# Performance work log

Measured on AMD Instinct MI355X. Metric: run time of the kernel, lower is better.

The kernel has to match this reference:

```python
import jax, jax.numpy as jnp
import numpy as np

L, B, E, H = 2048, 2, 1024, 16
HD = E // H


def setup_inputs() -> dict:
    key = jax.random.key(0)
    ks = jax.random.split(key, 5)
    s = 0.02
    return {
        "query": jax.random.normal(ks[0], (L, B, E), jnp.float32),
        "key": jax.random.normal(ks[1], (L, B, E), jnp.float32),
        "value": jax.random.normal(ks[2], (L, B, E), jnp.float32),
        "in_proj_weight": jax.random.normal(ks[3], (3 * E, E), jnp.float32) * s,
        "in_proj_bias": jnp.zeros((3 * E,), jnp.float32),
        "out_proj_weight": jax.random.normal(ks[4], (E, E), jnp.float32) * s,
        "out_proj_bias": jnp.zeros((E,), jnp.float32),
    }


def reference(query, key, value, in_proj_weight, in_proj_bias, out_proj_weight, out_proj_bias):
    # torch nn.MultiheadAttention math, seq-first [L, B, E], causal mask
    # (attend_mode='only_attend_front': positions j > i are masked).
    w_q, w_k, w_v = jnp.split(in_proj_weight, 3, axis=0)
    b_q, b_k, b_v = jnpp_split(in_proj_bias) if False else jnp.split(in_proj_bias, 3, axis=0)
    q = query @ w_q.T + b_q            # [L, B, E]
    k = key @ w_k.T + b_k
    v = value @ w_v.T + b_v

    def heads(x):  # [L, B, E] -> [B, H, L, HD]
        return x.reshape(x.shape[0], x.shape[1], H, HD).transpose(1, 2, 0, 3)

    qh, kh, vh = heads(q), heads(k), heads(v)
    scale = 1.0 / jnp.sqrt(jnp.asarray(HD, q.dtype))
    scores = jnp.einsum("bhqd,bhkd->bhqk", qh * scale, kh)  # [B, H, L, L]
    causal = jnp.triu(jnp.ones((scores.shape[-2], scores.shape[-1]), bool), k=1)
    scores = jnp.where(causal, jnp.asarray(-jnp.inf, scores.dtype), scores)
    attn = jax.nn.softmax(scores, axis=-1)
    out = jnp.einsum("bhqk,bhkd->bhqd", attn, vh)           # [B, H, L, HD]
    out = out.transpose(2, 0, 1, 3).reshape(query.shape[0], query.shape[1], E)  # [L, B, E]
    out = out @ out_proj_weight.T + out_proj_bias
    # torch also returns head-averaged attn weights [B, L, L]
    attn_avg = attn.mean(axis=1)
    return out, attn_avg
```

## Files before the change

kernel.cpp:

```cpp
#include <hip/hip_runtime.h>

#define L_ 2048
#define B_ 2
#define E_ 1024
#define H_ 16
#define HD_ 64
#define M_ 4096
#define K_ 1024

typedef unsigned short u16;
typedef unsigned int u32;
using short8  = __attribute__((ext_vector_type(8))) short;
using short4v = __attribute__((ext_vector_type(4))) short;
using floatx4 = __attribute__((ext_vector_type(4))) float;

__device__ inline u16 f2b(float f) {
  unsigned u = __float_as_uint(f);
  u += 0x7FFF + ((u >> 16) & 1);
  return (u16)(u >> 16);
}

__device__ inline u32 pack2(float a, float b) {
  u32 ua = __float_as_uint(a) + 0x8000u;
  u32 ub = __float_as_uint(b) + 0x8000u;
  return (ua >> 16) | (ub & 0xFFFF0000u);
}

__device__ inline floatx4 mfma16(short8 a, short8 b, floatx4 c) {
  return __builtin_amdgcn_mfma_f32_16x16x32_bf16(a, b, c, 0, 0, 0);
}

__device__ inline void gload16(const void* g, void* l) {
  __builtin_amdgcn_global_load_lds(
      (const __attribute__((address_space(1))) u32*)g,
      (__attribute__((address_space(3))) u32*)l, 16, 0, 0);
}

__global__ void convk(const float* __restrict__ src, u16* __restrict__ dst, int n4) {
  int i = blockIdx.x * blockDim.x + threadIdx.x;
  if (i < n4) {
    float4 v = ((const float4*)src)[i];
    ushort4 o;
    o.x = f2b(v.x); o.y = f2b(v.y); o.z = f2b(v.z); o.w = f2b(v.w);
    ((ushort4*)dst)[i] = o;
  }
}

template <int MODE>
__global__ __launch_bounds__(256) void gemm128(
    const u16* __restrict__ A, const u16* __restrict__ W, const float* __restrict__ bias,
    u16* __restrict__ qh, u16* __restrict__ kh, u16* __restrict__ vhT,
    float* __restrict__ outp)
{
  __shared__ __align__(16) u16 As[2][128 * 32];
  __shared__ __align__(16) u16 Bs[2][128 * 32];
  const int p = (MODE == 0) ? blockIdx.z : 0;
  const u16* Ap = A + (size_t)p * M_ * K_;
  const u16* Wp = W + (size_t)p * E_ * K_;
  const float* bp = bias + p * E_;
  const int row0 = blockIdx.y * 128, col0 = blockIdx.x * 128;
  const int t = threadIdx.x, lane = t & 63, wv = t >> 6;
  const int lanem = lane & 15, quad = lane >> 4;
  const int wm = wv >> 1, wn = wv & 1;

  int f0 = t, f1 = 256 + t;
  int r0s = f0 >> 2, q0s = (f0 & 3) ^ ((r0s >> 1) & 3);
  int r1s = f1 >> 2, q1s = (f1 & 3) ^ ((r1s >> 1) & 3);

  floatx4 acc[4][4];
#pragma unroll
  for (int mi = 0; mi < 4; ++mi)
#pragma unroll
    for (int ni = 0; ni < 4; ++ni) acc[mi][ni] = (floatx4){0.f, 0.f, 0.f, 0.f};

  const int swz = (lanem >> 1) & 3;

  auto STAGE = [&](int buf, int k0) {
    gload16(Ap + (size_t)(row0 + r0s) * K_ + k0 + q0s * 8, (char*)As[buf] + wv * 1024);
    gload16(Wp + (size_t)(col0 + r0s) * K_ + k0 + q0s * 8, (char*)Bs[buf] + wv * 1024);
    gload16(Ap + (size_t)(row0 + r1s) * K_ + k0 + q1s * 8, (char*)As[buf] + 4096 + wv * 1024);
    gload16(Wp + (size_t)(col0 + r1s) * K_ + k0 + q1s * 8, (char*)Bs[buf] + 4096 + wv * 1024);
  };

  STAGE(0, 0);
  for (int k0 = 0; k0 < K_; k0 += 32) {
    const int buf = (k0 >> 5) & 1;
    __syncthreads();
    if (k0 + 32 < K_) STAGE(buf ^ 1, k0 + 32);
    short8 af[4], bfg[4];
#pragma unroll
    for (int mi = 0; mi < 4; ++mi) {
      int r = wm * 64 + mi * 16 + lanem;
      af[mi] = *(const short8*)((const char*)As[buf] + r * 64 + (quad ^ swz) * 16);
    }
#pragma unroll
    for (int ni = 0; ni < 4; ++ni) {
      int r = wn * 64 + ni * 16 + lanem;
      bfg[ni] = *(const short8*)((const char*)Bs[buf] + r * 64 + (quad ^ swz) * 16);
    }
#pragma unroll
    for (int mi = 0; mi < 4; ++mi)
#pragma unroll
      for (int ni = 0; ni < 4; ++ni)
        acc[mi][ni] = mfma16(af[mi], bfg[ni], acc[mi][ni]);
  }

#pragma unroll
  for (int ni = 0; ni < 4; ++ni) {
    int gc = col0 + wn * 64 + ni * 16 + lanem;
    float bv = bp[gc];
#pragma unroll
    for (int mi = 0; mi < 4; ++mi) {
      int gr0 = row0 + wm * 64 + mi * 16 + quad * 4;
#pragma unroll
      for (int v = 0; v < 4; ++v) {
        float val = acc[mi][ni][v] + bv;
        int r = gr0 + v;
        if (MODE == 1) {
          outp[(size_t)r * E_ + gc] = val;
        } else {
          int l = r >> 1, bb = r & 1, hh = gc >> 6, d = gc & 63;
          u16 x = f2b(val);
          if (p == 0)      qh[(((size_t)bb * H_ + hh) * L_ + l) * HD_ + d] = x;
          else if (p == 1) kh[(((size_t)bb * H_ + hh) * L_ + l) * HD_ + d] = x;
          else {
            int lp = (l & ~31) | (((l >> 2) & 3) * 8 + ((l >> 4) & 1) * 4 + (l & 3));
            vhT[(((size_t)bb * H_ + hh) * HD_ + d) * L_ + lp] = x;
          }
        }
      }
    }
  }
}

__global__ __launch_bounds__(256, 2) void attn1(
    const u16* __restrict__ qh, const u16* __restrict__ kh, const u16* __restrict__ vhT,
    u16* __restrict__ ctx, float* __restrict__ li_ws)
{
  __shared__ __align__(16) u16 Ks[2][64 * 64];
  __shared__ __align__(16) u16 Vs[2][64 * 64];
  const int g = blockIdx.x;
  const int h = blockIdx.y, b = blockIdx.z;
  const int t = threadIdx.x, lane = t & 63, wv = t >> 6;
  const int lanem = lane & 15, quad = lane >> 4;
  const int bh = b * H_ + h;
  const int gB = (L_ / 64 - 1) - g;
  const int rowA = g * 64 + wv * 16 + lanem;
  const int rowB = gB * 64 + wv * 16 + lanem;

  const u16* qpA = qh + ((size_t)bh * L_ + rowA) * HD_;
  const u16* qpB = qh + ((size_t)bh * L_ + rowB) * HD_;
  short8 qA0 = *(const short8*)(qpA + quad * 8);
  short8 qA1 = *(const short8*)(qpA + 32 + quad * 8);
  short8 qB0 = *(const short8*)(qpB + quad * 8);
  short8 qB1 = *(const short8*)(qpB + 32 + quad * 8);

  const int srow = lane >> 3;
  const int spiece = (lane & 7) ^ srow;
  const u16* ksrc = kh + ((size_t)bh * L_ + wv * 16 + srow) * HD_ + spiece * 8;
  const u16* vsrc = vhT + ((size_t)bh * HD_ + wv * 16 + srow) * L_ + spiece * 8;

  const int ntiles = 32 - g;
  auto stage = [&](int buf) {
    gload16(ksrc, (char*)Ks[buf] + wv * 2048);
    gload16(ksrc + 8 * HD_, (char*)Ks[buf] + wv * 2048 + 1024);
    gload16(vsrc, (char*)Vs[buf] + wv * 2048);
    gload16(vsrc + (size_t)8 * L_, (char*)Vs[buf] + wv * 2048 + 1024);
    ksrc += 64 * HD_;
    vsrc += 64;
  };

  const int swz = lanem & 7;
  const int cb0 = lanem * 128 + ((quad ^ swz)) * 16;
  const int cb1 = lanem * 128 + ((quad ^ swz) ^ 4) * 16;

  float liA = 0.f, liB = 0.f;
  floatx4 oA[4], oB[4];
#pragma unroll
  for (int d = 0; d < 4; ++d) { oA[d] = (floatx4){0.f,0.f,0.f,0.f}; oB[d] = oA[d]; }

  int j0 = 0, tcur = 0;

  auto do_tile = [&](int modeA, int modeB) {
    __syncthreads();
    if (tcur + 1 < ntiles) stage((tcur + 1) & 1);
    const char* kbuf = (const char*)Ks[tcur & 1];
    const char* vbuf = (const char*)Vs[tcur & 1];

    floatx4 sA[4], sB[4];
#pragma unroll
    for (int jf = 0; jf < 4; ++jf) {
      short8 a0 = *(const short8*)(kbuf + cb0 + jf * 2048);
      short8 a1 = *(const short8*)(kbuf + cb1 + jf * 2048);
      floatx4 z = (floatx4){0.f,0.f,0.f,0.f};
      if (modeA != 2) sA[jf] = mfma16(a1, qA1, mfma16(a0, qA0, z));
      sB[jf] = mfma16(a1, qB1, mfma16(a0, qB0, z));
    }

    short8 pbA[2], pbB[2];
    auto soft = [&](floatx4* st, int row, float& li, short8* pb, int masked) {
#pragma unroll
      for (int jc = 0; jc < 2; ++jc) {
        float p[8];
#pragma unroll
        for (int r = 0; r < 4; ++r) {
          int ja = j0 + jc * 32 + quad * 4 + r;
          float e0 = __expf(st[jc * 2][r] * 0.125f);
          float e1 = __expf(st[jc * 2 + 1][r] * 0.125f);
          if (masked) {
            e0 = (ja <= row) ? e0 : 0.f;
            e1 = (ja + 16 <= row) ? e1 : 0.f;
          }
          li += e0 + e1;
          p[r] = e0; p[4 + r] = e1;
        }
        union { u32 w[4]; short8 s; } u;
        u.w[0] = pack2(p[0], p[1]); u.w[1] = pack2(p[2], p[3]);
        u.w[2] = pack2(p[4], p[5]); u.w[3] = pack2(p[6], p[7]);
        pb[jc] = u.s;
      }
    };
    if (modeA == 0) soft(sA, rowA, liA, pbA, 0);
    else if (modeA == 1) soft(sA, rowA, liA, pbA, 1);
    if (modeB == 0) soft(sB, rowB, liB, pbB, 0);
    else soft(sB, rowB, liB, pbB, 1);

#pragma unroll
    for (int jc = 0; jc < 2; ++jc) {
      const int base = (jc == 0) ? cb0 : cb1;
#pragma unroll
      for (int dbl = 0; dbl < 4; ++dbl) {
        short8 vf = *(const short8*)(vbuf + base + dbl * 2048);
        if (modeA != 2) oA[dbl] = mfma16(vf, pbA[jc], oA[dbl]);
        oB[dbl] = mfma16(vf, pbB[jc], oB[dbl]);
      }
    }
    j0 += 64;
    ++tcur;
  };

  stage(0);
  for (int jt = 0; jt < g; ++jt) do_tile(0, 0);
  do_tile(1, 0);
  for (int jt = g + 1; jt <= 30 - g; ++jt) do_tile(2, 0);
  do_tile(2, 1);

  liA += __shfl_xor(liA, 16); liA += __shfl_xor(liA, 32);
  liB += __shfl_xor(liB, 16); liB += __shfl_xor(liB, 32);
  float invA = 1.0f / liA, invB = 1.0f / liB;

  u16* cA = ctx + ((size_t)rowA * B_ + b) * E_ + h * HD_ + quad * 4;
  u16* cB = ctx + ((size_t)rowB * B_ + b) * E_ + h * HD_ + quad * 4;
#pragma unroll
  for (int dbl = 0; dbl < 4; ++dbl) {
    ushort4 pkA, pkB;
    pkA.x = f2b(oA[dbl][0] * invA); pkA.y = f2b(oA[dbl][1] * invA);
    pkA.z = f2b(oA[dbl][2] * invA); pkA.w = f2b(oA[dbl][3] * invA);
    pkB.x = f2b(oB[dbl][0] * invB); pkB.y = f2b(oB[dbl][1] * invB);
    pkB.z = f2b(oB[dbl][2] * invB); pkB.w = f2b(oB[dbl][3] * invB);
    *(ushort4*)(cA + dbl * 16) = pkA;
    *(ushort4*)(cB + dbl * 16) = pkB;
  }
  if (quad == 0) {
    li_ws[(size_t)bh * L_ + rowA] = invA;
    li_ws[(size_t)bh * L_ + rowB] = invB;
  }
}

__global__ __launch_bounds__(256, 2) void attn2(
    const u16* __restrict__ qh, const u16* __restrict__ kh,
    const float* __restrict__ li_ws, float* __restrict__ out2)
{
  __shared__ __align__(16) u16 Kb0[4][64 * 64];
  __shared__ __align__(16) u16 Kb1[4][64 * 64];
  const int jt = blockIdx.x, it = blockIdx.y, b = blockIdx.z;
  const int t = threadIdx.x, lane = t & 63, wv = t >> 6;
  const int lanem = lane & 15, quad = lane >> 4;
  const int j0 = jt * 64;
  const int i0 = it * 64;
  float* ob = out2 + (size_t)b * L_ * L_;

  if (jt > it) {
    float4 z = {0.f, 0.f, 0.f, 0.f};
    float* rp = ob + (size_t)(i0 + wv * 16 + lanem) * L_ + j0 + quad * 16;
    ((float4*)rp)[0] = z; ((float4*)rp)[1] = z;
    ((float4*)rp)[2] = z; ((float4*)rp)[3] = z;
    return;
  }

  const bool diag = (jt == it);
  const int srow = lane >> 3;
  const int spiece = (lane & 7) ^ srow;
  const int swz = lanem & 7;
  const int cb0 = lanem * 128 + ((quad ^ swz)) * 16;
  const int cb1 = lanem * 128 + (((4 + quad) ^ swz)) * 16;

  float acc[4][4][4] = {};

  auto STAGE = [&](u16* buf, int h) {
    const u16* kg = kh + ((size_t)(b * H_ + h) * L_ + j0) * HD_;
#pragma unroll
    for (int k = 0; k < 8; ++k)
      gload16(kg + (size_t)(k * 8 + srow) * HD_ + spiece * 8,
              (char*)buf + k * 1024);
  };

  short8 qc[4][2]; floatx4 lc[4];
  short8 qn[4][2]; floatx4 ln[4];
  auto LOADQ = [&](int h, short8 q[4][2], floatx4 l[4]) {
    const int bh = b * H_ + h;
#pragma unroll
    for (int mi = 0; mi < 4; ++mi) {
      const u16* qb = qh + ((size_t)bh * L_ + i0 + mi * 16 + lanem) * HD_;
      q[mi][0] = *(const short8*)(qb + quad * 8);
      q[mi][1] = *(const short8*)(qb + 32 + quad * 8);
      l[mi] = *(const floatx4*)(li_ws + (size_t)bh * L_ + i0 + mi * 16 + quad * 4);
    }
  };

  auto COMPUTE = [&](const u16* buf) {
#pragma unroll
    for (int mi = 0; mi < 4; ++mi) {
#pragma unroll
      for (int s = 0; s < 4; ++s) {
        if (diag && s > mi) continue;
        const char* kr = (const char*)buf + s * 2048;
        short8 b0 = *(const short8*)(kr + cb0);
        short8 b1 = *(const short8*)(kr + cb1);
        floatx4 sv = (floatx4){0.f, 0.f, 0.f, 0.f};
        sv = mfma16(qc[mi][0], b0, sv);
        sv = mfma16(qc[mi][1], b1, sv);
        if (!diag || s < mi) {
#pragma unroll
          for (int r = 0; r < 4; ++r)
            acc[mi][s][r] += __expf(sv[r] * 0.125f) * lc[mi][r];
        } else {
#pragma unroll
          for (int r = 0; r < 4; ++r)
            if (lanem <= quad * 4 + r)
              acc[mi][s][r] += __expf(sv[r] * 0.125f) * lc[mi][r];
        }
      }
    }
  };
  auto ROLL = [&]() {
#pragma unroll
    for (int mi = 0; mi < 4; ++mi) {
      qc[mi][0] = qn[mi][0]; qc[mi][1] = qn[mi][1]; lc[mi] = ln[mi];
    }
  };

  STAGE(Kb0[wv], wv);
  LOADQ(wv, qc, lc);

  STAGE(Kb1[wv], wv + 4);
  LOADQ(wv + 4, qn, ln);
  COMPUTE(Kb0[wv]);
  ROLL();

  STAGE(Kb0[wv], wv + 8);
  LOADQ(wv + 8, qn, ln);
  COMPUTE(Kb1[wv]);
  ROLL();

  STAGE(Kb1[wv], wv + 12);
  LOADQ(wv + 12, qn, ln);
  COMPUTE(Kb0[wv]);
  ROLL();

  COMPUTE(Kb1[wv]);

  {
    float* Plo = (float*)Kb0[wv];
    float* Phi = (float*)Kb1[wv];
#pragma unroll
    for (int mi = 0; mi < 4; ++mi) {
      float* P = (mi < 2) ? Plo : Phi;
      const int rbase = (mi & 1) * 16 + quad * 4;
#pragma unroll
      for (int s = 0; s < 4; ++s)
#pragma unroll
        for (int r = 0; r < 4; ++r)
          P[(rbase + r) * 64 + s * 16 + lanem] = acc[mi][s][r];
    }
  }
  __syncthreads();
#pragma unroll
  for (int rr = 0; rr < 4; ++rr) {
    const int rh = (wv & 1) * 16 + rr * 4 + quad;
    const int gi = i0 + wv * 16 + rr * 4 + quad;
    floatx4 ssum = (floatx4){0.f, 0.f, 0.f, 0.f};
#pragma unroll
    for (int p = 0; p < 4; ++p) {
      const float* P = (wv < 2) ? (const float*)Kb0[p] : (const float*)Kb1[p];
      ssum += *(const floatx4*)(P + rh * 64 + lanem * 4);
    }
    ssum *= (1.0f / H_);
    *(floatx4*)(ob + (size_t)gi * L_ + j0 + lanem * 4) = ssum;
  }
}

extern "C" void kernel_launch(void* const* d_in, const int* in_sizes, int n_in,
                              void* d_out, int out_size, void* d_ws, size_t ws_size,
                              hipStream_t stream) {
  const float* query = (const float*)d_in[0];
  const float* key   = (const float*)d_in[1];
  const float* value = (const float*)d_in[2];
  const float* w_in  = (const float*)d_in[3];
  const float* b_in  = (const float*)d_in[4];
  const float* w_out = (const float*)d_in[5];
  const float* b_out = (const float*)d_in[6];

  char* ws = (char*)d_ws;
  size_t off = 0;
  auto alloc = [&](size_t bytes) -> void* {
    void* p = ws + off;
    off += (bytes + 255) & ~(size_t)255;
    return p;
  };
  u16* w_in_b  = (u16*)alloc((size_t)3 * E_ * K_ * 2);
  u16* w_out_b = (u16*)alloc((size_t)E_ * K_ * 2);
  u16* x_b     = (u16*)alloc((size_t)3 * M_ * K_ * 2);
  u16* qh      = (u16*)alloc((size_t)B_ * H_ * L_ * HD_ * 2);
  u16* kh      = (u16*)alloc((size_t)B_ * H_ * L_ * HD_ * 2);
  u16* vhT     = (u16*)alloc((size_t)B_ * H_ * L_ * HD_ * 2);
  u16* ctx     = (u16*)alloc((size_t)M_ * E_ * 2);
  float* li_ws = (float*)alloc((size_t)B_ * H_ * L_ * 4);

  convk<<<4096, 256, 0, stream>>>(query, x_b + (size_t)0 * M_ * K_, M_ * K_ / 4);
  convk<<<4096, 256, 0, stream>>>(key,   x_b + (size_t)1 * M_ * K_, M_ * K_ / 4);
  convk<<<4096, 256, 0, stream>>>(value, x_b + (size_t)2 * M_ * K_, M_ * K_ / 4);
  convk<<<3072, 256, 0, stream>>>(w_in,  w_in_b,  3 * E_ * K_ / 4);
  convk<<<1024, 256, 0, stream>>>(w_out, w_out_b, E_ * K_ / 4);

  gemm128<0><<<dim3(E_ / 128, M_ / 128, 3), 256, 0, stream>>>(
      x_b, w_in_b, b_in, qh, kh, vhT, nullptr);

  attn1<<<dim3(L_ / 128, H_, B_), 256, 0, stream>>>(qh, kh, vhT, ctx, li_ws);

  attn2<<<dim3(L_ / 64, L_ / 64, B_), 256, 0, stream>>>(
      qh, kh, li_ws, (float*)d_out + (size_t)M_ * E_);

  gemm128<1><<<dim3(E_ / 128, M_ / 128, 1), 256, 0, stream>>>(
      ctx, w_out_b, b_out, nullptr, nullptr, nullptr, (float*)d_out);
}
```

Before: 277.7 us.

## Restructure head-averaged attention kernel to single-wave blocks looping over all heads

The attention-average kernel changes from four waves each handling four heads (reduced through shared memory with a barrier) to one 64-thread wave per 32x64 tile that loops over all 16 heads. It double-buffers K tiles with explicit vmcnt waits, so the cross-wave LDS reduction and barrier go away and the causal masking becomes finer-grained. The five fp32-to-bf16 conversion launches are also merged into one grid-z launch. The trade-off is many more small blocks, a longer serial loop per wave, and scalar rather than vectorized output stores.

```diff
diff --git a/kernel.cpp b/kernel.cpp
--- a/kernel.cpp
+++ b/kernel.cpp
@@ -36,12 +36,24 @@
       (__attribute__((address_space(3))) u32*)l, 16, 0, 0);
 }
 
-__global__ void convk(const float* __restrict__ src, u16* __restrict__ dst, int n4) {
+__global__ void convall(const float* __restrict__ q, const float* __restrict__ k,
+                        const float* __restrict__ v, const float* __restrict__ wi,
+                        const float* __restrict__ wo,
+                        u16* __restrict__ xb, u16* __restrict__ wib,
+                        u16* __restrict__ wob) {
+  const int z = blockIdx.z;
+  const float* src;
+  u16* dst;
+  int n4;
+  if (z < 3)      { src = (z == 0 ? q : (z == 1 ? k : v));
+                    dst = xb + (size_t)z * M_ * K_; n4 = M_ * K_ / 4; }
+  else if (z == 3){ src = wi; dst = wib; n4 = 3 * E_ * K_ / 4; }
+  else            { src = wo; dst = wob; n4 = E_ * K_ / 4; }
   int i = blockIdx.x * blockDim.x + threadIdx.x;
   if (i < n4) {
-    float4 v = ((const float4*)src)[i];
+    float4 val = ((const float4*)src)[i];
     ushort4 o;
-    o.x = f2b(v.x); o.y = f2b(v.y); o.z = f2b(v.z); o.w = f2b(v.w);
+    o.x = f2b(val.x); o.y = f2b(val.y); o.z = f2b(val.z); o.w = f2b(val.w);
     ((ushort4*)dst)[i] = o;
   }
 }
@@ -267,137 +279,126 @@
   }
 }
 
-__global__ __launch_bounds__(256, 2) void attn2(
+__global__ __launch_bounds__(64) void attn2(
     const u16* __restrict__ qh, const u16* __restrict__ kh,
     const float* __restrict__ li_ws, float* __restrict__ out2)
 {
-  __shared__ __align__(16) u16 Kb0[4][64 * 64];
-  __shared__ __align__(16) u16 Kb1[4][64 * 64];
-  const int jt = blockIdx.x, it = blockIdx.y, b = blockIdx.z;
-  const int t = threadIdx.x, lane = t & 63, wv = t >> 6;
+  __shared__ __align__(16) u16 KA[64 * 64];
+  __shared__ __align__(16) u16 KB[64 * 64];
+  const int jt = blockIdx.x, ig = blockIdx.y, b = blockIdx.z;
+  const int lane = threadIdx.x;
   const int lanem = lane & 15, quad = lane >> 4;
   const int j0 = jt * 64;
-  const int i0 = it * 64;
+  const int i0 = ig * 32;
   float* ob = out2 + (size_t)b * L_ * L_;
 
-  if (jt > it) {
+  if (j0 > i0 + 31) {
     float4 z = {0.f, 0.f, 0.f, 0.f};
-    float* rp = ob + (size_t)(i0 + wv * 16 + lanem) * L_ + j0 + quad * 16;
-    ((float4*)rp)[0] = z; ((float4*)rp)[1] = z;
-    ((float4*)rp)[2] = z; ((float4*)rp)[3] = z;
+    const int col = j0 + (lane & 15) * 4;
+#pragma unroll
+    for (int rr = 0; rr < 8; ++rr) {
+      int row = i0 + rr * 4 + (lane >> 4);
+      *(float4*)(ob + (size_t)row * L_ + col) = z;
+    }
     return;
   }
 
-  const bool diag = (jt == it);
   const int srow = lane >> 3;
   const int spiece = (lane & 7) ^ srow;
   const int swz = lanem & 7;
   const int cb0 = lanem * 128 + ((quad ^ swz)) * 16;
-  const int cb1 = lanem * 128 + (((4 + quad) ^ swz)) * 16;
-
-  float acc[4][4][4] = {};
+  const int cb1 = lanem * 128 + ((quad ^ swz) ^ 4) * 16;
+
+  float acc[2][4][4] = {};
 
   auto STAGE = [&](u16* buf, int h) {
     const u16* kg = kh + ((size_t)(b * H_ + h) * L_ + j0) * HD_;
 #pragma unroll
     for (int k = 0; k < 8; ++k)
-      gload16(kg + (size_t)(k * 8 + srow) * HD_ + spiece * 8,
-              (char*)buf + k * 1024);
-  };
-
-  short8 qc[4][2]; floatx4 lc[4];
-  short8 qn[4][2]; floatx4 ln[4];
-  auto LOADQ = [&](int h, short8 q[4][2], floatx4 l[4]) {
+      gload16(kg + (size_t)(k * 8 + srow) * HD_ + spiece * 8, (char*)buf + k * 1024);
+  };
+
+  short8 qc[4]; floatx4 lc[2];
+  short8 qn[4]; floatx4 ln[2];
+  auto LOADQ = [&](int h, short8 q[4], floatx4 l[2]) {
     const int bh = b * H_ + h;
-#pragma unroll
-    for (int mi = 0; mi < 4; ++mi) {
-      const u16* qb = qh + ((size_t)bh * L_ + i0 + mi * 16 + lanem) * HD_;
-      q[mi][0] = *(const short8*)(qb + quad * 8);
-      q[mi][1] = *(const short8*)(qb + 32 + quad * 8);
-      l[mi] = *(const floatx4*)(li_ws + (size_t)bh * L_ + i0 + mi * 16 + quad * 4);
-    }
+    const u16* qb0 = qh + ((size_t)bh * L_ + i0 + lanem) * HD_;
+    const u16* qb1 = qh + ((size_t)bh * L_ + i0 + 16 + lanem) * HD_;
+    q[0] = *(const short8*)(qb0 + quad * 8);
+    q[1] = *(const short8*)(qb0 + 32 + quad * 8);
+    q[2] = *(const short8*)(qb1 + quad * 8);
+    q[3] = *(const short8*)(qb1 + 32 + quad * 8);
+    l[0] = *(const floatx4*)(li_ws + (size_t)bh * L_ + i0 + quad * 4);
+    l[1] = *(const floatx4*)(li_ws + (size_t)bh * L_ + i0 + 16 + quad * 4);
   };
 
   auto COMPUTE = [&](const u16* buf) {
 #pragma unroll
-    for (int mi = 0; mi < 4; ++mi) {
+    for (int rg = 0; rg < 2; ++rg) {
+      const int rbase = i0 + rg * 16;
 #pragma unroll
       for (int s = 0; s < 4; ++s) {
-        if (diag && s > mi) continue;
+        if (j0 + s * 16 > rbase + 15) continue;
         const char* kr = (const char*)buf + s * 2048;
         short8 b0 = *(const short8*)(kr + cb0);
         short8 b1 = *(const short8*)(kr + cb1);
         floatx4 sv = (floatx4){0.f, 0.f, 0.f, 0.f};
-        sv = mfma16(qc[mi][0], b0, sv);
-        sv = mfma16(qc[mi][1], b1, sv);
-        if (!diag || s < mi) {
+        sv = mfma16(qc[rg * 2 + 0], b0, sv);
+        sv = mfma16(qc[rg * 2 + 1], b1, sv);
+        if (j0 + s * 16 + 15 <= rbase) {
 #pragma unroll
           for (int r = 0; r < 4; ++r)
-            acc[mi][s][r] += __expf(sv[r] * 0.125f) * lc[mi][r];
+            acc[rg][s][r] += __expf(sv[r] * 0.125f) * lc[rg][r];
         } else {
 #pragma unroll
-          for (int r = 0; r < 4; ++r)
-            if (lanem <= quad * 4 + r)
-              acc[mi][s][r] += __expf(sv[r] * 0.125f) * lc[mi][r];
+          for (int r = 0; r < 4; ++r) {
+            int irow = rbase + quad * 4 + r;
+            int jc = j0 + s * 16 + lanem;
+            if (jc <= irow) acc[rg][s][r] += __expf(sv[r] * 0.125f) * lc[rg][r];
+          }
         }
       }
     }
   };
   auto ROLL = [&]() {
 #pragma unroll
-    for (int mi = 0; mi < 4; ++mi) {
-      qc[mi][0] = qn[mi][0]; qc[mi][1] = qn[mi][1]; lc[mi] = ln[mi];
-    }
-  };
-
-  STAGE(Kb0[wv], wv);
-  LOADQ(wv, qc, lc);
-
-  STAGE(Kb1[wv], wv + 4);
-  LOADQ(wv + 4, qn, ln);
-  COMPUTE(Kb0[wv]);
+    for (int m = 0; m < 4; ++m) qc[m] = qn[m];
+    lc[0] = ln[0]; lc[1] = ln[1];
+  };
+
+  LOADQ(0, qc, lc);
+  STAGE(KA, 0);
+
+  for (int hp = 0; hp < 7; ++hp) {
+    LOADQ(2 * hp + 1, qn, ln);
+    STAGE(KB, 2 * hp + 1);
+    asm volatile("s_waitcnt vmcnt(14)" ::: "memory");
+    COMPUTE(KA);
+    ROLL();
+    LOADQ(2 * hp + 2, qn, ln);
+    STAGE(KA, 2 * hp + 2);
+    asm volatile("s_waitcnt vmcnt(14)" ::: "memory");
+    COMPUTE(KB);
+    ROLL();
+  }
+  LOADQ(15, qn, ln);
+  STAGE(KB, 15);
+  asm volatile("s_waitcnt vmcnt(14)" ::: "memory");
+  COMPUTE(KA);
   ROLL();
-
-  STAGE(Kb0[wv], wv + 8);
-  LOADQ(wv + 8, qn, ln);
-  COMPUTE(Kb1[wv]);
-  ROLL();
-
-  STAGE(Kb1[wv], wv + 12);
-  LOADQ(wv + 12, qn, ln);
-  COMPUTE(Kb0[wv]);
-  ROLL();
-
-  COMPUTE(Kb1[wv]);
-
-  {
-    float* Plo = (float*)Kb0[wv];
-    float* Phi = (float*)Kb1[wv];
-#pragma unroll
-    for (int mi = 0; mi < 4; ++mi) {
-      float* P = (mi < 2) ? Plo : Phi;
-      const int rbase = (mi & 1) * 16 + quad * 4;
-#pragma unroll
-      for (int s = 0; s < 4; ++s)
-#pragma unroll
-        for (int r = 0; r < 4; ++r)
-          P[(rbase + r) * 64 + s * 16 + lanem] = acc[mi][s][r];
-    }
-  }
-  __syncthreads();
-#pragma unroll
-  for (int rr = 0; rr < 4; ++rr) {
-    const int rh = (wv & 1) * 16 + rr * 4 + quad;
-    const int gi = i0 + wv * 16 + rr * 4 + quad;
-    floatx4 ssum = (floatx4){0.f, 0.f, 0.f, 0.f};
-#pragma unroll
-    for (int p = 0; p < 4; ++p) {
-      const float* P = (wv < 2) ? (const float*)Kb0[p] : (const float*)Kb1[p];
-      ssum += *(const floatx4*)(P + rh * 64 + lanem * 4);
-    }
-    ssum *= (1.0f / H_);
-    *(floatx4*)(ob + (size_t)gi * L_ + j0 + lanem * 4) = ssum;
-  }
+  asm volatile("s_waitcnt vmcnt(0)" ::: "memory");
+  COMPUTE(KB);
+
+#pragma unroll
+  for (int rg = 0; rg < 2; ++rg)
+#pragma unroll
+    for (int s = 0; s < 4; ++s)
+#pragma unroll
+      for (int r = 0; r < 4; ++r) {
+        int irow = i0 + rg * 16 + quad * 4 + r;
+        int jc = j0 + s * 16 + lanem;
+        ob[(size_t)irow * L_ + jc] = acc[rg][s][r] * (1.0f / H_);
+      }
 }
 
 extern "C" void kernel_launch(void* const* d_in, const int* in_sizes, int n_in,
@@ -427,18 +428,15 @@
   u16* ctx     = (u16*)alloc((size_t)M_ * E_ * 2);
   float* li_ws = (float*)alloc((size_t)B_ * H_ * L_ * 4);
 
-  convk<<<4096, 256, 0, stream>>>(query, x_b + (size_t)0 * M_ * K_, M_ * K_ / 4);
-  convk<<<4096, 256, 0, stream>>>(key,   x_b + (size_t)1 * M_ * K_, M_ * K_ / 4);
-  convk<<<4096, 256, 0, stream>>>(value, x_b + (size_t)2 * M_ * K_, M_ * K_ / 4);
-  convk<<<3072, 256, 0, stream>>>(w_in,  w_in_b,  3 * E_ * K_ / 4);
-  convk<<<1024, 256, 0, stream>>>(w_out, w_out_b, E_ * K_ / 4);
+  convall<<<dim3(4096, 1, 5), 256, 0, stream>>>(
+      query, key, value, w_in, w_out, x_b, w_in_b, w_out_b);
 
   gemm128<0><<<dim3(E_ / 128, M_ / 128, 3), 256, 0, stream>>>(
       x_b, w_in_b, b_in, qh, kh, vhT, nullptr);
 
   attn1<<<dim3(L_ / 128, H_, B_), 256, 0, stream>>>(qh, kh, vhT, ctx, li_ws);
 
-  attn2<<<dim3(L_ / 64, L_ / 64, B_), 256, 0, stream>>>(
+  attn2<<<dim3(L_ / 64, L_ / 32, B_), 64, 0, stream>>>(
       qh, kh, li_ws, (float*)d_out + (size_t)M_ * E_);
 
   gemm128<1><<<dim3(E_ / 128, M_ / 128, 1), 256, 0, stream>>>(
```

Measured after the change: 279.1 us. About the same (+0.5%).
